# Kernel optimization log

Measured on AMD Instinct MI355X. Metric: run time of the kernel, lower is better.

Reference implementation:

```python
import jax, jax.numpy as jnp
import numpy as np

B, N, D = 4, 256, 256
NEG = -1e9


def setup_inputs() -> dict:
    key = jax.random.key(0)
    k = jax.random.split(key, 5)
    scale1 = 1.0 / np.sqrt(4 * D)
    scale2 = 1.0 / np.sqrt(D)
    return {
        "shared": jax.random.normal(k[0], (B, N, D), dtype=jnp.float32),
        "W1": jax.random.uniform(k[1], (4 * D, D), jnp.float32, -scale1, scale1),
        "b1": jax.random.uniform(k[2], (D,), jnp.float32, -scale1, scale1),
        "W2": jax.random.uniform(k[3], (D, 1), jnp.float32, -scale2, scale2),
        "b2": jax.random.uniform(k[4], (1,), jnp.float32, -scale2, scale2),
    }


def reference(shared, W1, b1, W2, b2):
    # Linear on concat([src, tgt, |src-tgt|, src*tgt]) == sum of per-block matmuls.
    Wa, Wb, Wc, Wd = W1[:D], W1[D:2 * D], W1[2 * D:3 * D], W1[3 * D:]
    src_t = jnp.einsum('bid,dh->bih', shared, Wa)        # [B,N,D]
    tgt_t = jnp.einsum('bjd,dh->bjh', shared, Wb)        # [B,N,D]
    diff = jnp.abs(shared[:, :, None, :] - shared[:, None, :, :])  # [B,N,N,D]
    prod = shared[:, :, None, :] * shared[:, None, :, :]           # [B,N,N,D]
    h = (src_t[:, :, None, :] + tgt_t[:, None, :, :]
         + jnp.einsum('bijd,dh->bijh', diff, Wc)
         + jnp.einsum('bijd,dh->bijh', prod, Wd) + b1)   # [B,N,N,D]
    h = jax.nn.silu(h)
    scores = jnp.einsum('bijh,h->bij', h, W2[:, 0]) + b2[0]  # [B,N,N]
    eye = jnp.eye(N, dtype=bool)[None]
    scores = jnp.where(eye, NEG, scores)
    return jax.nn.softmax(scores, axis=-1)
```

## Files before the change

kernel.cpp:

```cpp
#include <hip/hip_runtime.h>

#define BB 4
#define NN 256
#define DD 256
#define HH 256
#define NEGV -1.0e9f

typedef _Float16 half8 __attribute__((ext_vector_type(8)));
typedef __fp16   fp16x2 __attribute__((ext_vector_type(2)));
typedef float floatx4 __attribute__((ext_vector_type(4)));

__global__ __launch_bounds__(256) void prep(const float* __restrict__ X,
                                            const float* __restrict__ W1,
                                            float* __restrict__ S,
                                            float* __restrict__ T,
                                            _Float16* __restrict__ Wst) {
  const int g = blockIdx.x;
  const int t = threadIdx.x;

  {
    const float wcv = W1[(size_t)(2 * DD + g) * HH + t];
    const float wdv = W1[(size_t)(3 * DD + g) * HH + t];
    const int ks = g >> 4;
    const int dd = g & 15;
    const int q  = dd >> 2;
    const int e  = (dd & 3) * 2;
    const int hgrp = t >> 4;
    const int ccw  = t & 15;
    _Float16* p = Wst + ((size_t)((ks * 16 + hgrp) * 4 + q) * 16 + ccw) * 8 + e;
    p[0] = (_Float16)wcv;
    p[1] = (_Float16)wdv;
  }

  const int row0 = g * 4;
  __shared__ float xr[4][256];
  {
    const float2* src2 = (const float2*)(X + (size_t)row0 * DD);
    float2* xr2 = (float2*)xr;
    xr2[t]       = src2[t];
    xr2[t + 256] = src2[t + 256];
  }
  __syncthreads();

  const int r2 = t >> 7;
  const int h  = (t & 127) * 2;
  const float* __restrict__ xA = xr[r2 * 2];
  const float* __restrict__ xB = xr[r2 * 2 + 1];
  float saAx = 0.f, saAy = 0.f, sbAx = 0.f, sbAy = 0.f;
  float saBx = 0.f, saBy = 0.f, sbBx = 0.f, sbBy = 0.f;
#pragma unroll 16
  for (int d = 0; d < 256; ++d) {
    const float2 wa = *(const float2*)&W1[(size_t)d * HH + h];
    const float2 wb = *(const float2*)&W1[(size_t)(DD + d) * HH + h];
    const float a = xA[d], c = xB[d];
    saAx = fmaf(a, wa.x, saAx); saAy = fmaf(a, wa.y, saAy);
    sbAx = fmaf(a, wb.x, sbAx); sbAy = fmaf(a, wb.y, sbAy);
    saBx = fmaf(c, wa.x, saBx); saBy = fmaf(c, wa.y, saBy);
    sbBx = fmaf(c, wb.x, sbBx); sbBy = fmaf(c, wb.y, sbBy);
  }
  const int rA = row0 + r2 * 2, rB = rA + 1;
  *(float2*)&S[(size_t)rA * HH + h] = make_float2(saAx, saAy);
  *(float2*)&S[(size_t)rB * HH + h] = make_float2(saBx, saBy);
  *(float2*)&T[(size_t)rA * HH + h] = make_float2(sbAx, sbAy);
  *(float2*)&T[(size_t)rB * HH + h] = make_float2(sbBx, sbBy);
}

__device__ __forceinline__ half8 make_afrag(const float4 xi, const float4 xj) {
  fp16x2 p0 = __builtin_amdgcn_cvt_pkrtz(__builtin_fabsf(xi.x - xj.x), xi.x * xj.x);
  fp16x2 p1 = __builtin_amdgcn_cvt_pkrtz(__builtin_fabsf(xi.y - xj.y), xi.y * xj.y);
  fp16x2 p2 = __builtin_amdgcn_cvt_pkrtz(__builtin_fabsf(xi.z - xj.z), xi.z * xj.z);
  fp16x2 p3 = __builtin_amdgcn_cvt_pkrtz(__builtin_fabsf(xi.w - xj.w), xi.w * xj.w);
  uint4 u;
  u.x = __builtin_bit_cast(unsigned int, p0);
  u.y = __builtin_bit_cast(unsigned int, p1);
  u.z = __builtin_bit_cast(unsigned int, p2);
  u.w = __builtin_bit_cast(unsigned int, p3);
  return __builtin_bit_cast(half8, u);
}

#define MFMA16(af, bf, acc) acc = __builtin_amdgcn_mfma_f32_16x16x32_f16(af, bf, acc, 0, 0, 0)

__global__ __launch_bounds__(512, 4) void score_mfma(
    const float* __restrict__ X,  const float* __restrict__ b1,
    const float* __restrict__ W2, const float* __restrict__ b2,
    const float* __restrict__ S,  const float* __restrict__ T,
    const _Float16* __restrict__ Wst, float* __restrict__ Sc) {

  const int beta = blockIdx.x;
  const int b    = blockIdx.y;
  int i, qt;
  if (beta < 64)       { qt = 0; i = beta; }
  else if (beta < 192) { qt = 1; i = beta - 64; }
  else if (beta < 384) { qt = 2; i = beta - 192; }
  else                 { qt = 3; i = beta - 384; }
  const int bi    = b * NN + i;
  const int jbase = qt * 64;
  const int isUp  = qt > (i >> 6);

  const int t     = threadIdx.x;
  const int lane  = t & 63;
  const int hg    = t >> 6;
  const int q     = lane >> 4;
  const int cc    = lane & 15;

  __shared__ __align__(16) float    xi_s[DD];
  __shared__ __align__(16) _Float16 Af[32768];
  __shared__ float pre_s[HH];
  __shared__ float pre2_s[HH];
  __shared__ float w2_s[HH];
  __shared__ float sc_s[8][64];

  if (t < 256) {
    xi_s[t]  = X[(size_t)bi * DD + t];
    pre_s[t] = S[(size_t)bi * HH + t] + b1[t];
  } else {
    const int u = t - 256;
    pre2_s[u] = T[(size_t)bi * HH + u] + b1[u];
    w2_s[u]   = W2[u];
  }

  const float* __restrict__ Tb = T + (size_t)b * NN * HH;
  const float* __restrict__ Sb = S + (size_t)b * NN * HH;

  const int jloc = t & 63;
  const int jg   = jloc >> 4;
  const int ccw  = jloc & 15;
  const float* __restrict__ xjrow = X + (size_t)(b * NN + jbase + jloc) * DD;

  const char* __restrict__ bsrc = (const char*)Wst + hg * 2048 + (size_t)lane * 16;

  half8 Bf0[4], Bf1[4];
#pragma unroll
  for (int u = 0; u < 4; ++u) {
    Bf0[u] = *(const half8*)(bsrc + (size_t)u * 16384);
    Bf1[u] = *(const half8*)(bsrc + (size_t)u * 16384 + 1024);
  }

  __syncthreads();

  {
    const int sgrp = t >> 6;
#pragma unroll
    for (int idx = 0; idx < 8; ++idx) {
      const int ksqg = sgrp * 8 + idx;
      const int d0   = ksqg * 4;
      const int kg   = ksqg >> 2;
      const int qw   = ksqg & 3;
      const float4 xi4 = *(const float4*)&xi_s[d0];
      const float4 xj4 = *(const float4*)(xjrow + d0);
      *(half8*)&Af[kg * 2048 + (jg * 4 + qw) * 128 + ccw * 8] = make_afrag(xi4, xj4);
    }
  }
  __syncthreads();

  floatx4 acc0[4], acc1[4];
#pragma unroll
  for (int u = 0; u < 4; ++u) { acc0[u] = (floatx4)0.f; acc1[u] = (floatx4)0.f; }

  const _Float16* ap0 = &Af[lane * 8];
  half8 An0 = *(const half8*)(ap0);
  half8 An1 = *(const half8*)(ap0 + 512);
  half8 An2 = *(const half8*)(ap0 + 1024);
  half8 An3 = *(const half8*)(ap0 + 1536);

#pragma unroll
  for (int kg = 0; kg < 16; ++kg) {
    const int s = kg & 3;
    const half8 Bc0 = Bf0[s], Bc1 = Bf1[s];
    const half8 Ac0 = An0, Ac1 = An1, Ac2 = An2, Ac3 = An3;
    if (kg < 12) {
      const char* bk = bsrc + (size_t)(kg + 4) * 16384;
      Bf0[s] = *(const half8*)(bk);
      Bf1[s] = *(const half8*)(bk + 1024);
    }
    if (kg < 15) {
      const _Float16* ap = &Af[(kg + 1) * 2048 + lane * 8];
      An0 = *(const half8*)(ap);
      An1 = *(const half8*)(ap + 512);
      An2 = *(const half8*)(ap + 1024);
      An3 = *(const half8*)(ap + 1536);
    }
    MFMA16(Ac0, Bc0, acc0[0]); MFMA16(Ac0, Bc1, acc1[0]);
    MFMA16(Ac1, Bc0, acc0[1]); MFMA16(Ac1, Bc1, acc1[1]);
    MFMA16(Ac2, Bc0, acc0[2]); MFMA16(Ac2, Bc1, acc1[2]);
    MFMA16(Ac3, Bc0, acc0[3]); MFMA16(Ac3, Bc1, acc1[3]);
  }

  const int h0   = hg * 32 + cc;
  const int h1   = h0 + 16;
  const int jrow = jbase + q * 4;

#define EPILOGUE(VROW, PRE) {                                                   \
    float tv0[16], tv1[16];                                                     \
    _Pragma("unroll")                                                           \
    for (int u = 0; u < 16; ++u) {                                              \
      const size_t j = (size_t)(jrow + (u >> 2) * 16 + (u & 3)) * HH;           \
      tv0[u] = VROW[j + h0];                                                    \
      tv1[u] = VROW[j + h1];                                                    \
    }                                                                           \
    const float w20 = w2_s[h0], pv0 = PRE[h0];                                  \
    const float w21 = w2_s[h1], pv1 = PRE[h1];                                  \
    float p[16];                                                                \
    _Pragma("unroll")                                                           \
    for (int u = 0; u < 16; ++u) {                                              \
      const float hv0 = acc0[u >> 2][u & 3] + pv0 + tv0[u];                     \
      const float sv0 = hv0 * __builtin_amdgcn_rcpf(1.f + __expf(-hv0));        \
      p[u] = sv0 * w20;                                                         \
      const float hv1 = acc1[u >> 2][u & 3] + pv1 + tv1[u];                     \
      const float sv1 = hv1 * __builtin_amdgcn_rcpf(1.f + __expf(-hv1));        \
      p[u] = fmaf(sv1, w21, p[u]);                                              \
    }                                                                           \
    _Pragma("unroll")                                                           \
    for (int u = 0; u < 16; ++u) {                                              \
      float v = p[u];                                                           \
      v += __shfl_xor(v, 1); v += __shfl_xor(v, 2);                             \
      v += __shfl_xor(v, 4); v += __shfl_xor(v, 8);                             \
      if (cc == 0) sc_s[hg][(u >> 2) * 16 + q * 4 + (u & 3)] = v;               \
    } }

  EPILOGUE(Tb, pre_s)
  __syncthreads();

  if (t < 64) {
    float s = sc_s[0][t] + sc_s[1][t] + sc_s[2][t] + sc_s[3][t]
            + sc_s[4][t] + sc_s[5][t] + sc_s[6][t] + sc_s[7][t] + b2[0];
    const int jg2 = jbase + t;
    if (jg2 == i) s = NEGV;
    Sc[(size_t)bi * NN + jg2] = s;
  }

  if (isUp) {
    __syncthreads();
    EPILOGUE(Sb, pre2_s)
    __syncthreads();
    if (t < 64) {
      const float s = sc_s[0][t] + sc_s[1][t] + sc_s[2][t] + sc_s[3][t]
                    + sc_s[4][t] + sc_s[5][t] + sc_s[6][t] + sc_s[7][t] + b2[0];
      Sc[(size_t)(b * NN + jbase + t) * NN + i] = s;
    }
  }
#undef EPILOGUE
}

__global__ __launch_bounds__(256) void softmax_kernel(const float* __restrict__ Sc,
                                                      float* __restrict__ out) {
  const int w    = threadIdx.x >> 6;
  const int lane = threadIdx.x & 63;
  const int bi   = blockIdx.x * 4 + w;
  const float4 v = *(const float4*)&Sc[(size_t)bi * NN + lane * 4];
  float m = fmaxf(fmaxf(v.x, v.y), fmaxf(v.z, v.w));
  m = fmaxf(m, __shfl_xor(m, 1));  m = fmaxf(m, __shfl_xor(m, 2));
  m = fmaxf(m, __shfl_xor(m, 4));  m = fmaxf(m, __shfl_xor(m, 8));
  m = fmaxf(m, __shfl_xor(m, 16)); m = fmaxf(m, __shfl_xor(m, 32));
  const float e0 = __expf(v.x - m), e1 = __expf(v.y - m);
  const float e2 = __expf(v.z - m), e3 = __expf(v.w - m);
  float sum = (e0 + e1) + (e2 + e3);
  sum += __shfl_xor(sum, 1);  sum += __shfl_xor(sum, 2);
  sum += __shfl_xor(sum, 4);  sum += __shfl_xor(sum, 8);
  sum += __shfl_xor(sum, 16); sum += __shfl_xor(sum, 32);
  const float r = 1.f / sum;
  float4 o; o.x = e0 * r; o.y = e1 * r; o.z = e2 * r; o.w = e3 * r;
  *(float4*)&out[(size_t)bi * NN + lane * 4] = o;
}

extern "C" void kernel_launch(void* const* d_in, const int* in_sizes, int n_in,
                              void* d_out, int out_size, void* d_ws, size_t ws_size,
                              hipStream_t stream) {
  const float* X  = (const float*)d_in[0];
  const float* W1 = (const float*)d_in[1];
  const float* b1 = (const float*)d_in[2];
  const float* W2 = (const float*)d_in[3];
  const float* b2 = (const float*)d_in[4];
  float* out = (float*)d_out;

  float*     Sws = (float*)d_ws;
  float*     Tws = Sws + (size_t)BB * NN * HH;
  _Float16*  Wst = (_Float16*)(Tws + (size_t)BB * NN * HH);
  float*     Scw = (float*)(Wst + (size_t)16 * HH * 32);

  prep<<<256, 256, 0, stream>>>(X, W1, Sws, Tws, Wst);
  score_mfma<<<dim3(640, BB), 512, 0, stream>>>(X, b1, W2, b2, Sws, Tws, Wst, Scw);
  softmax_kernel<<<BB * NN / 4, 256, 0, stream>>>(Scw, out);
}
```

Before: 162.8 us.

## Fuse prep, score and softmax into one persistent kernel with grid barriers

Replaces the three separate launches with a single persistent kernel of 512 blocks. Blocks split the prep work, synchronise through atomic grid barriers, loop over the score tiles, then run the softmax after a second barrier. This removes launch gaps and inter-kernel idle time. In exchange it adds a memset, relies on all 512 blocks being co-resident (risk of deadlock otherwise), and reloads the B fragments for every tile iteration.

```diff
diff --git a/kernel.cpp b/kernel.cpp
--- a/kernel.cpp
+++ b/kernel.cpp
@@ -5,65 +5,11 @@
 #define DD 256
 #define HH 256
 #define NEGV -1.0e9f
+#define GRID 512
 
 typedef _Float16 half8 __attribute__((ext_vector_type(8)));
 typedef __fp16   fp16x2 __attribute__((ext_vector_type(2)));
 typedef float floatx4 __attribute__((ext_vector_type(4)));
-
-__global__ __launch_bounds__(256) void prep(const float* __restrict__ X,
-                                            const float* __restrict__ W1,
-                                            float* __restrict__ S,
-                                            float* __restrict__ T,
-                                            _Float16* __restrict__ Wst) {
-  const int g = blockIdx.x;
-  const int t = threadIdx.x;
-
-  {
-    const float wcv = W1[(size_t)(2 * DD + g) * HH + t];
-    const float wdv = W1[(size_t)(3 * DD + g) * HH + t];
-    const int ks = g >> 4;
-    const int dd = g & 15;
-    const int q  = dd >> 2;
-    const int e  = (dd & 3) * 2;
-    const int hgrp = t >> 4;
-    const int ccw  = t & 15;
-    _Float16* p = Wst + ((size_t)((ks * 16 + hgrp) * 4 + q) * 16 + ccw) * 8 + e;
-    p[0] = (_Float16)wcv;
-    p[1] = (_Float16)wdv;
-  }
-
-  const int row0 = g * 4;
-  __shared__ float xr[4][256];
-  {
-    const float2* src2 = (const float2*)(X + (size_t)row0 * DD);
-    float2* xr2 = (float2*)xr;
-    xr2[t]       = src2[t];
-    xr2[t + 256] = src2[t + 256];
-  }
-  __syncthreads();
-
-  const int r2 = t >> 7;
-  const int h  = (t & 127) * 2;
-  const float* __restrict__ xA = xr[r2 * 2];
-  const float* __restrict__ xB = xr[r2 * 2 + 1];
-  float saAx = 0.f, saAy = 0.f, sbAx = 0.f, sbAy = 0.f;
-  float saBx = 0.f, saBy = 0.f, sbBx = 0.f, sbBy = 0.f;
-#pragma unroll 16
-  for (int d = 0; d < 256; ++d) {
-    const float2 wa = *(const float2*)&W1[(size_t)d * HH + h];
-    const float2 wb = *(const float2*)&W1[(size_t)(DD + d) * HH + h];
-    const float a = xA[d], c = xB[d];
-    saAx = fmaf(a, wa.x, saAx); saAy = fmaf(a, wa.y, saAy);
-    sbAx = fmaf(a, wb.x, sbAx); sbAy = fmaf(a, wb.y, sbAy);
-    saBx = fmaf(c, wa.x, saBx); saBy = fmaf(c, wa.y, saBy);
-    sbBx = fmaf(c, wb.x, sbBx); sbBy = fmaf(c, wb.y, sbBy);
-  }
-  const int rA = row0 + r2 * 2, rB = rA + 1;
-  *(float2*)&S[(size_t)rA * HH + h] = make_float2(saAx, saAy);
-  *(float2*)&S[(size_t)rB * HH + h] = make_float2(saBx, saBy);
-  *(float2*)&T[(size_t)rA * HH + h] = make_float2(sbAx, sbAy);
-  *(float2*)&T[(size_t)rB * HH + h] = make_float2(sbBx, sbBy);
-}
 
 __device__ __forceinline__ half8 make_afrag(const float4 xi, const float4 xj) {
   fp16x2 p0 = __builtin_amdgcn_cvt_pkrtz(__builtin_fabsf(xi.x - xj.x), xi.x * xj.x);
@@ -80,28 +26,28 @@
 
 #define MFMA16(af, bf, acc) acc = __builtin_amdgcn_mfma_f32_16x16x32_f16(af, bf, acc, 0, 0, 0)
 
-__global__ __launch_bounds__(512, 4) void score_mfma(
-    const float* __restrict__ X,  const float* __restrict__ b1,
-    const float* __restrict__ W2, const float* __restrict__ b2,
-    const float* __restrict__ S,  const float* __restrict__ T,
-    const _Float16* __restrict__ Wst, float* __restrict__ Sc) {
-
-  const int beta = blockIdx.x;
-  const int b    = blockIdx.y;
-  int i, qt;
-  if (beta < 64)       { qt = 0; i = beta; }
-  else if (beta < 192) { qt = 1; i = beta - 64; }
-  else if (beta < 384) { qt = 2; i = beta - 192; }
-  else                 { qt = 3; i = beta - 384; }
-  const int bi    = b * NN + i;
-  const int jbase = qt * 64;
-  const int isUp  = qt > (i >> 6);
-
-  const int t     = threadIdx.x;
-  const int lane  = t & 63;
-  const int hg    = t >> 6;
-  const int q     = lane >> 4;
-  const int cc    = lane & 15;
+__device__ __forceinline__ void grid_barrier(unsigned* c) {
+  __syncthreads();
+  if (threadIdx.x == 0) {
+    __threadfence();
+    __hip_atomic_fetch_add(c, 1u, __ATOMIC_ACQ_REL, __HIP_MEMORY_SCOPE_AGENT);
+    while (__hip_atomic_load(c, __ATOMIC_ACQUIRE, __HIP_MEMORY_SCOPE_AGENT) < GRID) {
+      __builtin_amdgcn_s_sleep(4);
+    }
+  }
+  __syncthreads();
+}
+
+__global__ __launch_bounds__(512, 4) void fused(
+    const float* __restrict__ X,  const float* __restrict__ W1,
+    const float* __restrict__ b1, const float* __restrict__ W2,
+    const float* __restrict__ b2,
+    float* __restrict__ S, float* __restrict__ T,
+    _Float16* __restrict__ Wst, float* __restrict__ Sc,
+    float* __restrict__ out, unsigned* __restrict__ bar) {
+
+  const int bid = blockIdx.x;
+  const int t   = threadIdx.x;
 
   __shared__ __align__(16) float    xi_s[DD];
   __shared__ __align__(16) _Float16 Af[32768];
@@ -110,157 +56,211 @@
   __shared__ float w2_s[HH];
   __shared__ float sc_s[8][64];
 
-  if (t < 256) {
-    xi_s[t]  = X[(size_t)bi * DD + t];
-    pre_s[t] = S[(size_t)bi * HH + t] + b1[t];
-  } else {
-    const int u = t - 256;
-    pre2_s[u] = T[(size_t)bi * HH + u] + b1[u];
-    w2_s[u]   = W2[u];
-  }
-
-  const float* __restrict__ Tb = T + (size_t)b * NN * HH;
-  const float* __restrict__ Sb = S + (size_t)b * NN * HH;
-
+  {
+    if (bid < 256) {
+      float* xstage = (float*)Af;
+      const int r0 = bid * 4;
+      xstage[t]       = X[(size_t)r0 * DD + t];
+      xstage[t + 512] = X[(size_t)r0 * DD + t + 512];
+      __syncthreads();
+      const int rr = t >> 7;
+      const int h  = (t & 127) * 2;
+      const float* __restrict__ xrow = xstage + rr * 256;
+      float sax = 0.f, say = 0.f, sbx = 0.f, sby = 0.f;
+#pragma unroll 8
+      for (int d = 0; d < 256; ++d) {
+        const float2 wa = *(const float2*)&W1[(size_t)d * HH + h];
+        const float2 wb = *(const float2*)&W1[(size_t)(DD + d) * HH + h];
+        const float x = xrow[d];
+        sax = fmaf(x, wa.x, sax); say = fmaf(x, wa.y, say);
+        sbx = fmaf(x, wb.x, sbx); sby = fmaf(x, wb.y, sby);
+      }
+      const int row = r0 + rr;
+      *(float2*)&S[(size_t)row * HH + h] = make_float2(sax, say);
+      *(float2*)&T[(size_t)row * HH + h] = make_float2(sbx, sby);
+    } else if (t < 256) {
+      const int g = bid - 256;
+      const float wcv = W1[(size_t)(2 * DD + g) * HH + t];
+      const float wdv = W1[(size_t)(3 * DD + g) * HH + t];
+      const int ks = g >> 4;
+      const int dd = g & 15;
+      const int q2 = dd >> 2;
+      const int e  = (dd & 3) * 2;
+      const int hgrp = t >> 4;
+      const int cw   = t & 15;
+      _Float16* p = Wst + ((size_t)((ks * 16 + hgrp) * 4 + q2) * 16 + cw) * 8 + e;
+      p[0] = (_Float16)wcv;
+      p[1] = (_Float16)wdv;
+    }
+  }
+  grid_barrier(bar);
+
+  const int lane = t & 63;
+  const int hg   = t >> 6;
+  const int q    = lane >> 4;
+  const int cc   = lane & 15;
   const int jloc = t & 63;
   const int jg   = jloc >> 4;
   const int ccw  = jloc & 15;
-  const float* __restrict__ xjrow = X + (size_t)(b * NN + jbase + jloc) * DD;
-
   const char* __restrict__ bsrc = (const char*)Wst + hg * 2048 + (size_t)lane * 16;
-
-  half8 Bf0[4], Bf1[4];
-#pragma unroll
-  for (int u = 0; u < 4; ++u) {
-    Bf0[u] = *(const half8*)(bsrc + (size_t)u * 16384);
-    Bf1[u] = *(const half8*)(bsrc + (size_t)u * 16384 + 1024);
-  }
-
-  __syncthreads();
-
-  {
-    const int sgrp = t >> 6;
-#pragma unroll
-    for (int idx = 0; idx < 8; ++idx) {
-      const int ksqg = sgrp * 8 + idx;
-      const int d0   = ksqg * 4;
-      const int kg   = ksqg >> 2;
-      const int qw   = ksqg & 3;
-      const float4 xi4 = *(const float4*)&xi_s[d0];
-      const float4 xj4 = *(const float4*)(xjrow + d0);
-      *(half8*)&Af[kg * 2048 + (jg * 4 + qw) * 128 + ccw * 8] = make_afrag(xi4, xj4);
-    }
-  }
-  __syncthreads();
-
-  floatx4 acc0[4], acc1[4];
-#pragma unroll
-  for (int u = 0; u < 4; ++u) { acc0[u] = (floatx4)0.f; acc1[u] = (floatx4)0.f; }
-
-  const _Float16* ap0 = &Af[lane * 8];
-  half8 An0 = *(const half8*)(ap0);
-  half8 An1 = *(const half8*)(ap0 + 512);
-  half8 An2 = *(const half8*)(ap0 + 1024);
-  half8 An3 = *(const half8*)(ap0 + 1536);
-
-#pragma unroll
-  for (int kg = 0; kg < 16; ++kg) {
-    const int s = kg & 3;
-    const half8 Bc0 = Bf0[s], Bc1 = Bf1[s];
-    const half8 Ac0 = An0, Ac1 = An1, Ac2 = An2, Ac3 = An3;
-    if (kg < 12) {
-      const char* bk = bsrc + (size_t)(kg + 4) * 16384;
-      Bf0[s] = *(const half8*)(bk);
-      Bf1[s] = *(const half8*)(bk + 1024);
-    }
-    if (kg < 15) {
-      const _Float16* ap = &Af[(kg + 1) * 2048 + lane * 8];
-      An0 = *(const half8*)(ap);
-      An1 = *(const half8*)(ap + 512);
-      An2 = *(const half8*)(ap + 1024);
-      An3 = *(const half8*)(ap + 1536);
-    }
-    MFMA16(Ac0, Bc0, acc0[0]); MFMA16(Ac0, Bc1, acc1[0]);
-    MFMA16(Ac1, Bc0, acc0[1]); MFMA16(Ac1, Bc1, acc1[1]);
-    MFMA16(Ac2, Bc0, acc0[2]); MFMA16(Ac2, Bc1, acc1[2]);
-    MFMA16(Ac3, Bc0, acc0[3]); MFMA16(Ac3, Bc1, acc1[3]);
-  }
-
-  const int h0   = hg * 32 + cc;
-  const int h1   = h0 + 16;
-  const int jrow = jbase + q * 4;
 
 #define EPILOGUE(VROW, PRE) {                                                   \
     float tv0[16], tv1[16];                                                     \
     _Pragma("unroll")                                                           \
-    for (int u = 0; u < 16; ++u) {                                              \
-      const size_t j = (size_t)(jrow + (u >> 2) * 16 + (u & 3)) * HH;           \
-      tv0[u] = VROW[j + h0];                                                    \
-      tv1[u] = VROW[j + h1];                                                    \
+    for (int u2 = 0; u2 < 16; ++u2) {                                           \
+      const size_t j = (size_t)(jrow + (u2 >> 2) * 16 + (u2 & 3)) * HH;         \
+      tv0[u2] = VROW[j + h0];                                                   \
+      tv1[u2] = VROW[j + h1];                                                   \
     }                                                                           \
     const float w20 = w2_s[h0], pv0 = PRE[h0];                                  \
     const float w21 = w2_s[h1], pv1 = PRE[h1];                                  \
     float p[16];                                                                \
     _Pragma("unroll")                                                           \
-    for (int u = 0; u < 16; ++u) {                                              \
-      const float hv0 = acc0[u >> 2][u & 3] + pv0 + tv0[u];                     \
+    for (int u2 = 0; u2 < 16; ++u2) {                                           \
+      const float hv0 = acc0[u2 >> 2][u2 & 3] + pv0 + tv0[u2];                  \
       const float sv0 = hv0 * __builtin_amdgcn_rcpf(1.f + __expf(-hv0));        \
-      p[u] = sv0 * w20;                                                         \
-      const float hv1 = acc1[u >> 2][u & 3] + pv1 + tv1[u];                     \
+      p[u2] = sv0 * w20;                                                        \
+      const float hv1 = acc1[u2 >> 2][u2 & 3] + pv1 + tv1[u2];                  \
       const float sv1 = hv1 * __builtin_amdgcn_rcpf(1.f + __expf(-hv1));        \
-      p[u] = fmaf(sv1, w21, p[u]);                                              \
+      p[u2] = fmaf(sv1, w21, p[u2]);                                            \
     }                                                                           \
     _Pragma("unroll")                                                           \
-    for (int u = 0; u < 16; ++u) {                                              \
-      float v = p[u];                                                           \
+    for (int u2 = 0; u2 < 16; ++u2) {                                           \
+      float v = p[u2];                                                          \
       v += __shfl_xor(v, 1); v += __shfl_xor(v, 2);                             \
       v += __shfl_xor(v, 4); v += __shfl_xor(v, 8);                             \
-      if (cc == 0) sc_s[hg][(u >> 2) * 16 + q * 4 + (u & 3)] = v;               \
+      if (cc == 0) sc_s[hg][(u2 >> 2) * 16 + q * 4 + (u2 & 3)] = v;             \
     } }
 
-  EPILOGUE(Tb, pre_s)
-  __syncthreads();
-
-  if (t < 64) {
-    float s = sc_s[0][t] + sc_s[1][t] + sc_s[2][t] + sc_s[3][t]
-            + sc_s[4][t] + sc_s[5][t] + sc_s[6][t] + sc_s[7][t] + b2[0];
-    const int jg2 = jbase + t;
-    if (jg2 == i) s = NEGV;
-    Sc[(size_t)bi * NN + jg2] = s;
-  }
-
-  if (isUp) {
-    __syncthreads();
-    EPILOGUE(Sb, pre2_s)
-    __syncthreads();
+  for (int u = bid; u < 640 * BB; u += GRID) {
+    const int beta = u % 640;
+    const int b    = u / 640;
+    int i, qt;
+    if (beta < 64)       { qt = 0; i = beta; }
+    else if (beta < 192) { qt = 1; i = beta - 64; }
+    else if (beta < 384) { qt = 2; i = beta - 192; }
+    else                 { qt = 3; i = beta - 384; }
+    const int bi    = b * NN + i;
+    const int jbase = qt * 64;
+    const int isUp  = qt > (i >> 6);
+
+    __syncthreads();
+    if (t < 256) {
+      xi_s[t]  = X[(size_t)bi * DD + t];
+      pre_s[t] = S[(size_t)bi * HH + t] + b1[t];
+    } else {
+      const int uu = t - 256;
+      pre2_s[uu] = T[(size_t)bi * HH + uu] + b1[uu];
+      w2_s[uu]   = W2[uu];
+    }
+
+    const float* __restrict__ Tb = T + (size_t)b * NN * HH;
+    const float* __restrict__ Sb = S + (size_t)b * NN * HH;
+    const float* __restrict__ xjrow = X + (size_t)(b * NN + jbase + jloc) * DD;
+
+    half8 Bf0[4], Bf1[4];
+#pragma unroll
+    for (int v = 0; v < 4; ++v) {
+      Bf0[v] = *(const half8*)(bsrc + (size_t)v * 16384);
+      Bf1[v] = *(const half8*)(bsrc + (size_t)v * 16384 + 1024);
+    }
+
+    __syncthreads();
+
+    {
+      const int sgrp = t >> 6;
+#pragma unroll
+      for (int idx = 0; idx < 8; ++idx) {
+        const int ksqg = sgrp * 8 + idx;
+        const int d0   = ksqg * 4;
+        const int kg   = ksqg >> 2;
+        const int qw   = ksqg & 3;
+        const float4 xi4 = *(const float4*)&xi_s[d0];
+        const float4 xj4 = *(const float4*)(xjrow + d0);
+        *(half8*)&Af[kg * 2048 + (jg * 4 + qw) * 128 + ccw * 8] = make_afrag(xi4, xj4);
+      }
+    }
+    __syncthreads();
+
+    floatx4 acc0[4], acc1[4];
+#pragma unroll
+    for (int v = 0; v < 4; ++v) { acc0[v] = (floatx4)0.f; acc1[v] = (floatx4)0.f; }
+
+    const _Float16* ap0 = &Af[lane * 8];
+    half8 An0 = *(const half8*)(ap0);
+    half8 An1 = *(const half8*)(ap0 + 512);
+    half8 An2 = *(const half8*)(ap0 + 1024);
+    half8 An3 = *(const half8*)(ap0 + 1536);
+
+#pragma unroll
+    for (int kg = 0; kg < 16; ++kg) {
+      const int s = kg & 3;
+      const half8 Bc0 = Bf0[s], Bc1 = Bf1[s];
+      const half8 Ac0 = An0, Ac1 = An1, Ac2 = An2, Ac3 = An3;
+      if (kg < 12) {
+        const char* bk = bsrc + (size_t)(kg + 4) * 16384;
+        Bf0[s] = *(const half8*)(bk);
+        Bf1[s] = *(const half8*)(bk + 1024);
+      }
+      if (kg < 15) {
+        const _Float16* ap = &Af[(kg + 1) * 2048 + lane * 8];
+        An0 = *(const half8*)(ap);
+        An1 = *(const half8*)(ap + 512);
+        An2 = *(const half8*)(ap + 1024);
+        An3 = *(const half8*)(ap + 1536);
+      }
+      MFMA16(Ac0, Bc0, acc0[0]); MFMA16(Ac0, Bc1, acc1[0]);
+      MFMA16(Ac1, Bc0, acc0[1]); MFMA16(Ac1, Bc1, acc1[1]);
+      MFMA16(Ac2, Bc0, acc0[2]); MFMA16(Ac2, Bc1, acc1[2]);
+      MFMA16(Ac3, Bc0, acc0[3]); MFMA16(Ac3, Bc1, acc1[3]);
+    }
+
+    const int h0   = hg * 32 + cc;
+    const int h1   = h0 + 16;
+    const int jrow = jbase + q * 4;
+
+    EPILOGUE(Tb, pre_s)
+    __syncthreads();
+
     if (t < 64) {
-      const float s = sc_s[0][t] + sc_s[1][t] + sc_s[2][t] + sc_s[3][t]
-                    + sc_s[4][t] + sc_s[5][t] + sc_s[6][t] + sc_s[7][t] + b2[0];
-      Sc[(size_t)(b * NN + jbase + t) * NN + i] = s;
+      float s = sc_s[0][t] + sc_s[1][t] + sc_s[2][t] + sc_s[3][t]
+              + sc_s[4][t] + sc_s[5][t] + sc_s[6][t] + sc_s[7][t] + b2[0];
+      const int jg2 = jbase + t;
+      if (jg2 == i) s = NEGV;
+      Sc[(size_t)bi * NN + jg2] = s;
+    }
+
+    if (isUp) {
+      __syncthreads();
+      EPILOGUE(Sb, pre2_s)
+      __syncthreads();
+      if (t < 64) {
+        const float s = sc_s[0][t] + sc_s[1][t] + sc_s[2][t] + sc_s[3][t]
+                      + sc_s[4][t] + sc_s[5][t] + sc_s[6][t] + sc_s[7][t] + b2[0];
+        Sc[(size_t)(b * NN + jbase + t) * NN + i] = s;
+      }
     }
   }
 #undef EPILOGUE
-}
-
-__global__ __launch_bounds__(256) void softmax_kernel(const float* __restrict__ Sc,
-                                                      float* __restrict__ out) {
-  const int w    = threadIdx.x >> 6;
-  const int lane = threadIdx.x & 63;
-  const int bi   = blockIdx.x * 4 + w;
-  const float4 v = *(const float4*)&Sc[(size_t)bi * NN + lane * 4];
-  float m = fmaxf(fmaxf(v.x, v.y), fmaxf(v.z, v.w));
-  m = fmaxf(m, __shfl_xor(m, 1));  m = fmaxf(m, __shfl_xor(m, 2));
-  m = fmaxf(m, __shfl_xor(m, 4));  m = fmaxf(m, __shfl_xor(m, 8));
-  m = fmaxf(m, __shfl_xor(m, 16)); m = fmaxf(m, __shfl_xor(m, 32));
-  const float e0 = __expf(v.x - m), e1 = __expf(v.y - m);
-  const float e2 = __expf(v.z - m), e3 = __expf(v.w - m);
-  float sum = (e0 + e1) + (e2 + e3);
-  sum += __shfl_xor(sum, 1);  sum += __shfl_xor(sum, 2);
-  sum += __shfl_xor(sum, 4);  sum += __shfl_xor(sum, 8);
-  sum += __shfl_xor(sum, 16); sum += __shfl_xor(sum, 32);
-  const float r = 1.f / sum;
-  float4 o; o.x = e0 * r; o.y = e1 * r; o.z = e2 * r; o.w = e3 * r;
-  *(float4*)&out[(size_t)bi * NN + lane * 4] = o;
+  grid_barrier(bar + 1);
+
+  for (int u = bid; u < (BB * NN) / 8; u += GRID) {
+    const int bi = u * 8 + hg;
+    const float4 v = *(const float4*)&Sc[(size_t)bi * NN + lane * 4];
+    float m = fmaxf(fmaxf(v.x, v.y), fmaxf(v.z, v.w));
+    m = fmaxf(m, __shfl_xor(m, 1));  m = fmaxf(m, __shfl_xor(m, 2));
+    m = fmaxf(m, __shfl_xor(m, 4));  m = fmaxf(m, __shfl_xor(m, 8));
+    m = fmaxf(m, __shfl_xor(m, 16)); m = fmaxf(m, __shfl_xor(m, 32));
+    const float e0 = __expf(v.x - m), e1 = __expf(v.y - m);
+    const float e2 = __expf(v.z - m), e3 = __expf(v.w - m);
+    float sum = (e0 + e1) + (e2 + e3);
+    sum += __shfl_xor(sum, 1);  sum += __shfl_xor(sum, 2);
+    sum += __shfl_xor(sum, 4);  sum += __shfl_xor(sum, 8);
+    sum += __shfl_xor(sum, 16); sum += __shfl_xor(sum, 32);
+    const float r = 1.f / sum;
+    float4 o; o.x = e0 * r; o.y = e1 * r; o.z = e2 * r; o.w = e3 * r;
+    *(float4*)&out[(size_t)bi * NN + lane * 4] = o;
+  }
 }
 
 extern "C" void kernel_launch(void* const* d_in, const int* in_sizes, int n_in,
@@ -277,8 +277,10 @@
   float*     Tws = Sws + (size_t)BB * NN * HH;
   _Float16*  Wst = (_Float16*)(Tws + (size_t)BB * NN * HH);
   float*     Scw = (float*)(Wst + (size_t)16 * HH * 32);
-
-  prep<<<256, 256, 0, stream>>>(X, W1, Sws, Tws, Wst);
-  score_mfma<<<dim3(640, BB), 512, 0, stream>>>(X, b1, W2, b2, Sws, Tws, Wst, Scw);
-  softmax_kernel<<<BB * NN / 4, 256, 0, stream>>>(Scw, out);
-}
+  unsigned*  bar = (unsigned*)(Scw + (size_t)BB * NN * NN);
+
+  hipMemsetAsync(bar, 0, 2 * sizeof(unsigned), stream);
+
+  fused<<<GRID, 512, 0, stream>>>(X, W1, b1, W2, b2,
+                                  Sws, Tws, Wst, Scw, out, bar);
+}
```

New measurement: 393.3 us. 2.42x slower.
